# Optimization experiments

Measured on AMD Instinct MI355X. Metric: run time of the kernel, lower is better.

## Reference

```python
import jax, jax.numpy as jnp
import numpy as np

EMB = 1024  # embedding_size in the torch module


def setup_inputs() -> dict:
    key = jax.random.key(0)
    ks = jax.random.split(key, 6)
    B, N, K = 64, 256, 4096
    y = jax.random.normal(ks[0], (B, N, 1024), dtype=jnp.float32)
    # nn.Linear weights, init normal(std=0.02), zero bias
    Wy_w = jax.random.normal(ks[1], (1024, 1024), dtype=jnp.float32) * 0.02  # [out,in]
    Wy_b = jnp.zeros((1024,), dtype=jnp.float32)
    Wz_w = jax.random.normal(ks[2], (1024, 2048), dtype=jnp.float32) * 0.02  # [out,in]
    Wz_b = jnp.zeros((1024,), dtype=jnp.float32)
    dic_z = jax.random.normal(ks[3], (K, 2048), dtype=jnp.float32)
    prior = jax.random.uniform(ks[4], (K,), dtype=jnp.float32)
    prior = prior / jnp.sum(prior)
    return {"y": y, "Wy_w": Wy_w, "Wy_b": Wy_b, "Wz_w": Wz_w, "Wz_b": Wz_b,
            "dic_z": dic_z, "prior": prior}


def reference(y, Wy_w, Wy_b, Wz_w, Wz_b, dic_z, prior):
    # h = Wy(y): [B,N,1024]; dz = Wz(dic_z): [K,1024]
    h = jnp.einsum('bni,oi->bno', y, Wy_w) + Wy_b
    dz = jnp.einsum('ki,oi->ko', dic_z, Wz_w) + Wz_b
    # attention over dictionary: [B,N,K]
    att = jax.nn.softmax(jnp.einsum('bnd,kd->bnk', h, dz) / jnp.sqrt(jnp.float32(EMB)), axis=-1)
    # z[b,n] = sum_k prior[k] * att[b,n,k] * dic_z[k]  -> [B,N,2048]
    # (avoids the [B,N,K,2048] intermediate the torch code materializes)
    z = jnp.einsum('bnk,k,ke->bne', att, prior, dic_z)
    return z
```

## Files before the change

### kernel.cpp

```cpp
#include <hip/hip_runtime.h>
#include <hip/hip_bf16.h>
#include <stdint.h>

typedef __bf16 bf16;
typedef __bf16 bf16x4 __attribute__((ext_vector_type(4)));
typedef __bf16 bf16x8 __attribute__((ext_vector_type(8)));
typedef float f32x4 __attribute__((ext_vector_type(4)));
typedef unsigned short ushort8 __attribute__((ext_vector_type(8)));

__device__ __forceinline__ void gload16(const bf16* g, char* l) {
  __builtin_amdgcn_global_load_lds(
      reinterpret_cast<const __attribute__((address_space(1))) unsigned int*>(
          reinterpret_cast<uintptr_t>(g)),
      reinterpret_cast<__attribute__((address_space(3))) unsigned int*>(
          reinterpret_cast<uintptr_t>(l)),
      16, 0, 0);
}

#define VMCNT(n)  asm volatile("s_waitcnt vmcnt(" #n ")" ::: "memory")
#define LGKM0()   do { asm volatile("s_waitcnt lgkmcnt(0)" ::: "memory"); \
                       __builtin_amdgcn_sched_barrier(0); } while (0)
#define BAR()     __builtin_amdgcn_s_barrier()

#define CAST_B 2048
__global__ __launch_bounds__(256) void prep_all(
    const float* __restrict__ y, bf16* __restrict__ yo, int na,
    const float* __restrict__ wy, bf16* __restrict__ wyo, int nb,
    const float* __restrict__ wz, bf16* __restrict__ wzo, int nc,
    const float* __restrict__ dic, const float* __restrict__ prior,
    bf16* __restrict__ dicb, bf16* __restrict__ w3t) {
  __shared__ bf16 t[64][72];
  const int tid = threadIdx.x;
  if ((int)blockIdx.x < CAST_B) {
    int i = blockIdx.x * 256 + tid;
    const int stride = CAST_B * 256;
    const int tot = na + nb + nc;
    for (; i < tot; i += stride) {
      const float* src; bf16* dst; int j;
      if (i < na)            { src = y;  dst = yo;  j = i; }
      else if (i < na + nb)  { src = wy; dst = wyo; j = i - na; }
      else                   { src = wz; dst = wzo; j = i - na - nb; }
      const float4 v0 = reinterpret_cast<const float4*>(src)[j * 2];
      const float4 v1 = reinterpret_cast<const float4*>(src)[j * 2 + 1];
      bf16x8 o = { (bf16)v0.x, (bf16)v0.y, (bf16)v0.z, (bf16)v0.w,
                   (bf16)v1.x, (bf16)v1.y, (bf16)v1.z, (bf16)v1.w };
      reinterpret_cast<bf16x8*>(dst)[j] = o;
    }
  } else {
    const int KD = 4096, E = 2048;
    const int b2 = blockIdx.x - CAST_B;
    const int k0 = (b2 & 63) * 64, e0 = (b2 >> 6) * 64;
    const int er = (tid & 15) * 4;
    const int kr = tid >> 4;
#pragma unroll
    for (int p = 0; p < 4; ++p) {
      const int k = kr + p * 16;
      const float pr = prior[k0 + k];
      const float4 v = *reinterpret_cast<const float4*>(dic + (size_t)(k0 + k) * E + e0 + er);
      bf16x4 db = { (bf16)v.x, (bf16)v.y, (bf16)v.z, (bf16)v.w };
      *reinterpret_cast<bf16x4*>(dicb + (size_t)(k0 + k) * E + e0 + er) = db;
      t[er + 0][k] = (bf16)(v.x * pr);
      t[er + 1][k] = (bf16)(v.y * pr);
      t[er + 2][k] = (bf16)(v.z * pr);
      t[er + 3][k] = (bf16)(v.w * pr);
    }
    __syncthreads();
    const int e = tid >> 2, kc = (tid & 3) * 16;
    ushort8 a = *reinterpret_cast<ushort8*>(&t[e][kc]);
    ushort8 b = *reinterpret_cast<ushort8*>(&t[e][kc + 8]);
    unsigned short* dst = (unsigned short*)w3t + (size_t)(e0 + e) * KD + k0 + kc;
    *reinterpret_cast<ushort8*>(dst) = a;
    *reinterpret_cast<ushort8*>(dst + 8) = b;
  }
}

__global__ __launch_bounds__(256) void rowsum_bf16(const unsigned short* __restrict__ S,
                                                   float* __restrict__ sums) {
  const int row = blockIdx.x * 4 + (threadIdx.x >> 6);
  const int lane = threadIdx.x & 63;
  const unsigned short* r = S + (size_t)row * 4096;
  float s = 0.f;
#pragma unroll
  for (int i = 0; i < 8; ++i) {
    ushort8 v = *reinterpret_cast<const ushort8*>(r + i * 512 + lane * 8);
#pragma unroll
    for (int j = 0; j < 8; ++j) s += __uint_as_float(((unsigned)v[j]) << 16);
  }
#pragma unroll
  for (int o = 32; o; o >>= 1) s += __shfl_xor(s, o);
  if (lane == 0) sums[row] = s;
}

template <int EPI, int BN>
__device__ __forceinline__ void gemm_body(
    const bf16* __restrict__ A, const bf16* __restrict__ B,
    const float* __restrict__ aux, float* __restrict__ psum,
    void* __restrict__ Cout, int M, int N, int K, float scale, int nparts,
    int orig, int nwg, char* lds) {
  constexpr int BUFSZ = 32768 + BN * 128;
  constexpr int BOFF = 32768;
  constexpr int TM = (BN == 256) ? 128 : 64;
  constexpr int MI = TM / 16;
  constexpr int NI = 4;
  const int tid = threadIdx.x;
  const int lane = tid & 63, w = tid >> 6;

  const int gridN = N / BN;
  int wgid;
  { const int q = nwg >> 3, r = nwg & 7, x = orig & 7, rest = orig >> 3;
    wgid = (x < r ? x * (q + 1) : r * (q + 1) + (x - r) * q) + rest; }
  const int m0 = (wgid / gridN) * 256;
  const int n0 = (wgid % gridN) * BN;

  const int srow = lane >> 3;
  const int scol = ((lane & 7) ^ srow) * 8;
  const bf16* gA = A + (size_t)(m0 + w * 8 + srow) * K + scol;
  const bf16* gB = B + (size_t)(n0 + w * 8 + srow) * K + scol;

  auto stA = [&](char* dst, int u, int h) {
    gload16(gA + (size_t)(h * 128) * K + (size_t)u * 64, dst + h * 16384 + w * 1024);
    gload16(gA + (size_t)(h * 128 + 64) * K + (size_t)u * 64, dst + h * 16384 + 8192 + w * 1024);
  };
  auto stB = [&](char* dst, int u, int h) {
    gload16(gB + (size_t)(h * 128) * K + (size_t)u * 64, dst + BOFF + h * 16384 + w * 1024);
    gload16(gB + (size_t)(h * 128 + 64) * K + (size_t)u * 64, dst + BOFF + h * 16384 + 8192 + w * 1024);
  };

  const int fr = lane & 15, hi = lane >> 4;
  int wm, wn;
  if constexpr (BN == 256) { wm = w >> 2; wn = w & 3; }
  else                     { wm = w >> 1; wn = w & 1; }
  const int abase = (wm * TM + fr) * 128 + ((hi ^ (fr & 7)) << 4);
  const int bbase = BOFF + (wn * 64 + fr) * 128 + ((hi ^ (fr & 7)) << 4);
#define RD_A(b, mi, ks) (*(const bf16x8*)((b) + ((abase + (mi) * 2048) ^ ((ks) << 6))))
#define RD_B(b, ni, ks) (*(const bf16x8*)((b) + ((bbase + (ni) * 2048) ^ ((ks) << 6))))

  f32x4 acc[MI][NI] = {};
  const int NT = K >> 6;

  stA(lds, 0, 0); stA(lds, 0, 1);
  stB(lds, 0, 0);
  if constexpr (BN == 256) stB(lds, 0, 1);
  stB(lds + BUFSZ, 1, 0);
  if constexpr (BN == 256) { stB(lds + BUFSZ, 1, 1); VMCNT(4); }
  else                     { VMCNT(2); }
  BAR();

  for (int u = 0; u < NT; ++u) {
    char* b  = lds + (size_t)(u & 1) * BUFSZ;
    char* bn = lds + (size_t)((u + 1) & 1) * BUFSZ;
    bf16x8 bb[2][NI], a[2][2];
    const bool sA = (u + 1) < NT, sB = (u + 2) < NT;

    if constexpr (BN == 256) {
      a[0][0] = RD_A(b, 0, 0); a[0][1] = RD_A(b, 0, 1);
      a[1][0] = RD_A(b, 1, 0); a[1][1] = RD_A(b, 1, 1);
#pragma unroll
      for (int ni = 0; ni < NI; ++ni) { bb[0][ni] = RD_B(b, ni, 0); bb[1][ni] = RD_B(b, ni, 1); }
      if (sA) stA(bn, u + 1, 0);
      LGKM0();
#pragma unroll
      for (int m2 = 0; m2 < 2; ++m2)
#pragma unroll
        for (int ni = 0; ni < NI; ++ni) {
          acc[m2][ni] = __builtin_amdgcn_mfma_f32_16x16x32_bf16(a[m2][0], bb[0][ni], acc[m2][ni], 0, 0, 0);
          acc[m2][ni] = __builtin_amdgcn_mfma_f32_16x16x32_bf16(a[m2][1], bb[1][ni], acc[m2][ni], 0, 0, 0);
        }
      a[0][0] = RD_A(b, 2, 0); a[0][1] = RD_A(b, 2, 1);
      a[1][0] = RD_A(b, 3, 0); a[1][1] = RD_A(b, 3, 1);
      if (sA) stA(bn, u + 1, 1);
      LGKM0();
#pragma unroll
      for (int m2 = 0; m2 < 2; ++m2)
#pragma unroll
        for (int ni = 0; ni < NI; ++ni) {
          acc[2 + m2][ni] = __builtin_amdgcn_mfma_f32_16x16x32_bf16(a[m2][0], bb[0][ni], acc[2 + m2][ni], 0, 0, 0);
          acc[2 + m2][ni] = __builtin_amdgcn_mfma_f32_16x16x32_bf16(a[m2][1], bb[1][ni], acc[2 + m2][ni], 0, 0, 0);
        }
      BAR();
      a[0][0] = RD_A(b, 4, 0); a[0][1] = RD_A(b, 4, 1);
      a[1][0] = RD_A(b, 5, 0); a[1][1] = RD_A(b, 5, 1);
      if (sB) stB(b, u + 2, 0);
      LGKM0();
#pragma unroll
      for (int m2 = 0; m2 < 2; ++m2)
#pragma unroll
        for (int ni = 0; ni < NI; ++ni) {
          acc[4 + m2][ni] = __builtin_amdgcn_mfma_f32_16x16x32_bf16(a[m2][0], bb[0][ni], acc[4 + m2][ni], 0, 0, 0);
          acc[4 + m2][ni] = __builtin_amdgcn_mfma_f32_16x16x32_bf16(a[m2][1], bb[1][ni], acc[4 + m2][ni], 0, 0, 0);
        }
      a[0][0] = RD_A(b, 6, 0); a[0][1] = RD_A(b, 6, 1);
      a[1][0] = RD_A(b, 7, 0); a[1][1] = RD_A(b, 7, 1);
      if (sB) stB(b, u + 2, 1);
      if (sB) VMCNT(4); else VMCNT(0);
      LGKM0();
#pragma unroll
      for (int m2 = 0; m2 < 2; ++m2)
#pragma unroll
        for (int ni = 0; ni < NI; ++ni) {
          acc[6 + m2][ni] = __builtin_amdgcn_mfma_f32_16x16x32_bf16(a[m2][0], bb[0][ni], acc[6 + m2][ni], 0, 0, 0);
          acc[6 + m2][ni] = __builtin_amdgcn_mfma_f32_16x16x32_bf16(a[m2][1], bb[1][ni], acc[6 + m2][ni], 0, 0, 0);
        }
      BAR();
    } else {
      a[0][0] = RD_A(b, 0, 0); a[0][1] = RD_A(b, 0, 1);
      a[1][0] = RD_A(b, 1, 0); a[1][1] = RD_A(b, 1, 1);
#pragma unroll
      for (int ni = 0; ni < NI; ++ni) { bb[0][ni] = RD_B(b, ni, 0); bb[1][ni] = RD_B(b, ni, 1); }
      if (sA) { stA(bn, u + 1, 0); stA(bn, u + 1, 1); }
      LGKM0();
      __builtin_amdgcn_s_setprio(1);
#pragma unroll
      for (int m2 = 0; m2 < 2; ++m2)
#pragma unroll
        for (int ni = 0; ni < NI; ++ni) {
          acc[m2][ni] = __builtin_amdgcn_mfma_f32_16x16x32_bf16(a[m2][0], bb[0][ni], acc[m2][ni], 0, 0, 0);
          acc[m2][ni] = __builtin_amdgcn_mfma_f32_16x16x32_bf16(a[m2][1], bb[1][ni], acc[m2][ni], 0, 0, 0);
        }
      __builtin_amdgcn_s_setprio(0);
      BAR();
      a[0][0] = RD_A(b, 2, 0); a[0][1] = RD_A(b, 2, 1);
      a[1][0] = RD_A(b, 3, 0); a[1][1] = RD_A(b, 3, 1);
      if (sB) stB(b, u + 2, 0);
      if (sB) VMCNT(2); else VMCNT(0);
      LGKM0();
      __builtin_amdgcn_s_setprio(1);
#pragma unroll
      for (int m2 = 0; m2 < 2; ++m2)
#pragma unroll
        for (int ni = 0; ni < NI; ++ni) {
          acc[2 + m2][ni] = __builtin_amdgcn_mfma_f32_16x16x32_bf16(a[m2][0], bb[0][ni], acc[2 + m2][ni], 0, 0, 0);
          acc[2 + m2][ni] = __builtin_amdgcn_mfma_f32_16x16x32_bf16(a[m2][1], bb[1][ni], acc[2 + m2][ni], 0, 0, 0);
        }
      __builtin_amdgcn_s_setprio(0);
      BAR();
    }
  }
#undef RD_A
#undef RD_B

  float* lsum = (float*)lds;
  if constexpr (EPI == 2) {
    if (tid < 256) {
      const float* p = aux + (size_t)(m0 + tid) * nparts;
      float s = 0.f;
      for (int bp = 0; bp < nparts; ++bp) s += p[bp];
      lsum[tid] = s;
    }
    __syncthreads();
  }

  const int lro = hi * 4;
  if constexpr (EPI == 2) {
#pragma unroll
    for (int mi = 0; mi < MI; ++mi)
#pragma unroll
      for (int j = 0; j < 4; ++j) {
        const int lr = wm * TM + mi * 16 + lro + j;
        const float inv = 1.0f / lsum[lr];
        const size_t grow = (size_t)(m0 + lr) * N;
#pragma unroll
        for (int ni = 0; ni < NI; ++ni)
          ((float*)Cout)[grow + n0 + wn * 64 + ni * 16 + fr] = acc[mi][ni][j] * inv;
      }
  } else {
    float rs[MI][4];
    if constexpr (EPI == 1) {
#pragma unroll
      for (int mi = 0; mi < MI; ++mi)
#pragma unroll
        for (int j = 0; j < 4; ++j) rs[mi][j] = 0.f;
    }
#pragma unroll
    for (int ni = 0; ni < NI; ++ni) {
      const int gcol = n0 + wn * 64 + ni * 16 + fr;
      float bvs = 0.f;
      if constexpr (EPI == 0) bvs = aux[gcol];
#pragma unroll
      for (int mi = 0; mi < MI; ++mi) {
        const int grow = m0 + wm * TM + mi * 16 + lro;
#pragma unroll
        for (int j = 0; j < 4; ++j) {
          float c = acc[mi][ni][j] * scale + bvs;
          if constexpr (EPI == 1) { c = __expf(c); rs[mi][j] += c; }
          ((bf16*)Cout)[(size_t)(grow + j) * N + gcol] = (bf16)c;
        }
      }
    }
    if constexpr (EPI == 1) {
      if (psum != nullptr) {
        float* wsum = (float*)lds;
        __syncthreads();
#pragma unroll
        for (int mi = 0; mi < MI; ++mi)
#pragma unroll
          for (int j = 0; j < 4; ++j) {
            float s = rs[mi][j];
            s += __shfl_xor(s, 1); s += __shfl_xor(s, 2);
            s += __shfl_xor(s, 4); s += __shfl_xor(s, 8);
            if (fr == 0) wsum[wn * 256 + wm * TM + mi * 16 + lro + j] = s;
          }
        __syncthreads();
        if (tid < 256) {
          const float s = wsum[tid] + wsum[256 + tid] + wsum[512 + tid] + wsum[768 + tid];
          psum[(size_t)(m0 + tid) * 16 + (n0 >> 8)] = s;
        }
      }
    }
  }
}

template <int EPI, int BN>
__global__ __launch_bounds__(512, 2) void gemm8(
    const bf16* __restrict__ A, const bf16* __restrict__ B,
    const float* __restrict__ aux, float* __restrict__ psum,
    void* __restrict__ Cout, int M, int N, int K, float scale, int nparts) {
  extern __shared__ char lds[];
  gemm_body<EPI, BN>(A, B, aux, psum, Cout, M, N, K, scale, nparts,
                     blockIdx.x, gridDim.x, lds);
}

__global__ __launch_bounds__(512, 2) void gemm_g23(
    const bf16* __restrict__ A2, const bf16* __restrict__ B2,
    const float* __restrict__ b2, bf16* __restrict__ C2,
    const bf16* __restrict__ A3, const bf16* __restrict__ B3,
    const float* __restrict__ b3, bf16* __restrict__ C3,
    int M, int D, int E, int KD, int g2n) {
  extern __shared__ char lds[];
  if ((int)blockIdx.x < g2n)
    gemm_body<0, 256>(A2, B2, b2, nullptr, C2, M, D, D, 1.0f, 0,
                      blockIdx.x, g2n, lds);
  else
    gemm_body<0, 128>(A3, B3, b3, nullptr, C3, KD, D, E, 1.0f, 0,
                      blockIdx.x - g2n, gridDim.x - g2n, lds);
}

extern "C" void kernel_launch(void* const* d_in, const int* in_sizes, int n_in,
                              void* d_out, int out_size, void* d_ws, size_t ws_size,
                              hipStream_t stream) {
  const float* y     = (const float*)d_in[0];
  const float* Wy_w  = (const float*)d_in[1];
  const float* Wy_b  = (const float*)d_in[2];
  const float* Wz_w  = (const float*)d_in[3];
  const float* Wz_b  = (const float*)d_in[4];
  const float* dic   = (const float*)d_in[5];
  const float* prior = (const float*)d_in[6];
  float* z = (float*)d_out;

  const int M = 16384, D = 1024, E = 2048, KD = 4096;

  char* ws = (char*)d_ws;
  bf16* w3t  = (bf16*)(ws);
  bf16* h    = (bf16*)(ws + ((size_t)16 << 20));
  bf16* dzb  = (bf16*)(ws + ((size_t)48 << 20));
  bf16* S    = (bf16*)(ws + ((size_t)56 << 20));
  bf16* yb   = (bf16*)(ws + ((size_t)56 << 20));
  bf16* Wyb  = (bf16*)(ws + ((size_t)88 << 20));
  bf16* Wzb  = (bf16*)(ws + ((size_t)90 << 20));
  bf16* dicb = (bf16*)(ws + ((size_t)94 << 20));

  const bool fused_sum = ws_size >= ((size_t)185 << 20);
  float* psum = fused_sum ? (float*)(ws + ((size_t)184 << 20)) : nullptr;
  float* sums = (float*)(ws + ((size_t)16 << 20));

  prep_all<<<CAST_B + 2048, 256, 0, stream>>>(
      y, yb, M * D / 8, Wy_w, Wyb, D * D / 8, Wz_w, Wzb, D * E / 8,
      dic, prior, dicb, w3t);
  {
    const int g2n = (M / 256) * (D / 256);
    const int g3n = (KD / 256) * (D / 128);
    gemm_g23<<<g2n + g3n, 512, 131072, stream>>>(
        yb, Wyb, Wy_b, h, dicb, Wzb, Wz_b, dzb, M, D, E, KD, g2n);
  }
  gemm8<1, 256><<<(M / 256) * (KD / 256), 512, 131072, stream>>>(
      h, dzb, nullptr, psum, S, M, KD, D, 0.03125f, 0);
  if (!fused_sum) {
    rowsum_bf16<<<M / 4, 256, 0, stream>>>((const unsigned short*)S, sums);
  }
  gemm8<2, 256><<<(M / 256) * (E / 256), 512, 131072, stream>>>(
      S, w3t, fused_sum ? psum : sums, nullptr, z, M, E, KD, 1.0f,
      fused_sum ? 16 : 1);
}
```

Baseline: 490.4 us.

## Triple-buffer B tiles in LDS to remove one barrier per k-step

Restructures the GEMM LDS layout so A uses a two-stage ring and B uses a separate three-stage ring indexed by u%3. B prefetches for step u+2 no longer overwrite the buffer being read, which lets the mid-iteration barrier be dropped, leaving one barrier per k-tile. It also removes the s_setprio hints in the BN=128 path. Dynamic LDS grows to 160 KB per workgroup, which stays within one workgroup per CU but adds more LDS address arithmetic (modulo 3).

```diff
diff --git a/kernel.cpp b/kernel.cpp
--- a/kernel.cpp
+++ b/kernel.cpp
@@ -97,8 +97,8 @@
     const float* __restrict__ aux, float* __restrict__ psum,
     void* __restrict__ Cout, int M, int N, int K, float scale, int nparts,
     int orig, int nwg, char* lds) {
-  constexpr int BUFSZ = 32768 + BN * 128;
-  constexpr int BOFF = 32768;
+  constexpr int BSZ = BN * 128;
+  constexpr int BBASE = 65536;
   constexpr int TM = (BN == 256) ? 128 : 64;
   constexpr int MI = TM / 16;
   constexpr int NI = 4;
@@ -117,13 +117,15 @@
   const bf16* gA = A + (size_t)(m0 + w * 8 + srow) * K + scol;
   const bf16* gB = B + (size_t)(n0 + w * 8 + srow) * K + scol;
 
-  auto stA = [&](char* dst, int u, int h) {
-    gload16(gA + (size_t)(h * 128) * K + (size_t)u * 64, dst + h * 16384 + w * 1024);
-    gload16(gA + (size_t)(h * 128 + 64) * K + (size_t)u * 64, dst + h * 16384 + 8192 + w * 1024);
+  auto stA = [&](int u, int h) {
+    char* dst = lds + (size_t)(u & 1) * 32768 + h * 16384;
+    gload16(gA + (size_t)(h * 128) * K + (size_t)u * 64, dst + w * 1024);
+    gload16(gA + (size_t)(h * 128 + 64) * K + (size_t)u * 64, dst + 8192 + w * 1024);
   };
-  auto stB = [&](char* dst, int u, int h) {
-    gload16(gB + (size_t)(h * 128) * K + (size_t)u * 64, dst + BOFF + h * 16384 + w * 1024);
-    gload16(gB + (size_t)(h * 128 + 64) * K + (size_t)u * 64, dst + BOFF + h * 16384 + 8192 + w * 1024);
+  auto stB = [&](int u, int h) {
+    char* dst = lds + BBASE + (size_t)(u % 3) * BSZ + h * 16384;
+    gload16(gB + (size_t)(h * 128) * K + (size_t)u * 64, dst + w * 1024);
+    gload16(gB + (size_t)(h * 128 + 64) * K + (size_t)u * 64, dst + 8192 + w * 1024);
   };
 
   const int fr = lane & 15, hi = lane >> 4;
@@ -131,33 +133,35 @@
   if constexpr (BN == 256) { wm = w >> 2; wn = w & 3; }
   else                     { wm = w >> 1; wn = w & 1; }
   const int abase = (wm * TM + fr) * 128 + ((hi ^ (fr & 7)) << 4);
-  const int bbase = BOFF + (wn * 64 + fr) * 128 + ((hi ^ (fr & 7)) << 4);
-#define RD_A(b, mi, ks) (*(const bf16x8*)((b) + ((abase + (mi) * 2048) ^ ((ks) << 6))))
-#define RD_B(b, ni, ks) (*(const bf16x8*)((b) + ((bbase + (ni) * 2048) ^ ((ks) << 6))))
+  const int bbase = (wn * 64 + fr) * 128 + ((hi ^ (fr & 7)) << 4);
+#define RD_A(ab, mi, ks) (*(const bf16x8*)((ab) + ((abase + (mi) * 2048) ^ ((ks) << 6))))
+#define RD_B(bp, ni, ks) (*(const bf16x8*)((bp) + ((bbase + (ni) * 2048) ^ ((ks) << 6))))
 
   f32x4 acc[MI][NI] = {};
   const int NT = K >> 6;
 
-  stA(lds, 0, 0); stA(lds, 0, 1);
-  stB(lds, 0, 0);
-  if constexpr (BN == 256) stB(lds, 0, 1);
-  stB(lds + BUFSZ, 1, 0);
-  if constexpr (BN == 256) { stB(lds + BUFSZ, 1, 1); VMCNT(4); }
-  else                     { VMCNT(2); }
+  stA(0, 0); stA(0, 1);
+  if constexpr (BN == 256) {
+    stB(0, 0); stB(0, 1); stB(1, 0); stB(1, 1);
+    VMCNT(4);
+  } else {
+    stB(0, 0); stB(1, 0);
+    VMCNT(2);
+  }
   BAR();
 
   for (int u = 0; u < NT; ++u) {
-    char* b  = lds + (size_t)(u & 1) * BUFSZ;
-    char* bn = lds + (size_t)((u + 1) & 1) * BUFSZ;
+    const char* ab = lds + (size_t)(u & 1) * 32768;
+    const char* bp = lds + BBASE + (size_t)(u % 3) * BSZ;
     bf16x8 bb[2][NI], a[2][2];
     const bool sA = (u + 1) < NT, sB = (u + 2) < NT;
 
     if constexpr (BN == 256) {
-      a[0][0] = RD_A(b, 0, 0); a[0][1] = RD_A(b, 0, 1);
-      a[1][0] = RD_A(b, 1, 0); a[1][1] = RD_A(b, 1, 1);
-#pragma unroll
-      for (int ni = 0; ni < NI; ++ni) { bb[0][ni] = RD_B(b, ni, 0); bb[1][ni] = RD_B(b, ni, 1); }
-      if (sA) stA(bn, u + 1, 0);
+      a[0][0] = RD_A(ab, 0, 0); a[0][1] = RD_A(ab, 0, 1);
+      a[1][0] = RD_A(ab, 1, 0); a[1][1] = RD_A(ab, 1, 1);
+#pragma unroll
+      for (int ni = 0; ni < NI; ++ni) { bb[0][ni] = RD_B(bp, ni, 0); bb[1][ni] = RD_B(bp, ni, 1); }
+      if (sA) stA(u + 1, 0);
       LGKM0();
 #pragma unroll
       for (int m2 = 0; m2 < 2; ++m2)
@@ -166,9 +170,9 @@
           acc[m2][ni] = __builtin_amdgcn_mfma_f32_16x16x32_bf16(a[m2][0], bb[0][ni], acc[m2][ni], 0, 0, 0);
           acc[m2][ni] = __builtin_amdgcn_mfma_f32_16x16x32_bf16(a[m2][1], bb[1][ni], acc[m2][ni], 0, 0, 0);
         }
-      a[0][0] = RD_A(b, 2, 0); a[0][1] = RD_A(b, 2, 1);
-      a[1][0] = RD_A(b, 3, 0); a[1][1] = RD_A(b, 3, 1);
-      if (sA) stA(bn, u + 1, 1);
+      a[0][0] = RD_A(ab, 2, 0); a[0][1] = RD_A(ab, 2, 1);
+      a[1][0] = RD_A(ab, 3, 0); a[1][1] = RD_A(ab, 3, 1);
+      if (sA) stA(u + 1, 1);
       LGKM0();
 #pragma unroll
       for (int m2 = 0; m2 < 2; ++m2)
@@ -177,10 +181,9 @@
           acc[2 + m2][ni] = __builtin_amdgcn_mfma_f32_16x16x32_bf16(a[m2][0], bb[0][ni], acc[2 + m2][ni], 0, 0, 0);
           acc[2 + m2][ni] = __builtin_amdgcn_mfma_f32_16x16x32_bf16(a[m2][1], bb[1][ni], acc[2 + m2][ni], 0, 0, 0);
         }
-      BAR();
-      a[0][0] = RD_A(b, 4, 0); a[0][1] = RD_A(b, 4, 1);
-      a[1][0] = RD_A(b, 5, 0); a[1][1] = RD_A(b, 5, 1);
-      if (sB) stB(b, u + 2, 0);
+      a[0][0] = RD_A(ab, 4, 0); a[0][1] = RD_A(ab, 4, 1);
+      a[1][0] = RD_A(ab, 5, 0); a[1][1] = RD_A(ab, 5, 1);
+      if (sB) stB(u + 2, 0);
       LGKM0();
 #pragma unroll
       for (int m2 = 0; m2 < 2; ++m2)
@@ -189,9 +192,9 @@
           acc[4 + m2][ni] = __builtin_amdgcn_mfma_f32_16x16x32_bf16(a[m2][0], bb[0][ni], acc[4 + m2][ni], 0, 0, 0);
           acc[4 + m2][ni] = __builtin_amdgcn_mfma_f32_16x16x32_bf16(a[m2][1], bb[1][ni], acc[4 + m2][ni], 0, 0, 0);
         }
-      a[0][0] = RD_A(b, 6, 0); a[0][1] = RD_A(b, 6, 1);
-      a[1][0] = RD_A(b, 7, 0); a[1][1] = RD_A(b, 7, 1);
-      if (sB) stB(b, u + 2, 1);
+      a[0][0] = RD_A(ab, 6, 0); a[0][1] = RD_A(ab, 6, 1);
+      a[1][0] = RD_A(ab, 7, 0); a[1][1] = RD_A(ab, 7, 1);
+      if (sB) stB(u + 2, 1);
       if (sB) VMCNT(4); else VMCNT(0);
       LGKM0();
 #pragma unroll
@@ -203,13 +206,12 @@
         }
       BAR();
     } else {
-      a[0][0] = RD_A(b, 0, 0); a[0][1] = RD_A(b, 0, 1);
-      a[1][0] = RD_A(b, 1, 0); a[1][1] = RD_A(b, 1, 1);
-#pragma unroll
-      for (int ni = 0; ni < NI; ++ni) { bb[0][ni] = RD_B(b, ni, 0); bb[1][ni] = RD_B(b, ni, 1); }
-      if (sA) { stA(bn, u + 1, 0); stA(bn, u + 1, 1); }
-      LGKM0();
-      __builtin_amdgcn_s_setprio(1);
+      a[0][0] = RD_A(ab, 0, 0); a[0][1] = RD_A(ab, 0, 1);
+      a[1][0] = RD_A(ab, 1, 0); a[1][1] = RD_A(ab, 1, 1);
+#pragma unroll
+      for (int ni = 0; ni < NI; ++ni) { bb[0][ni] = RD_B(bp, ni, 0); bb[1][ni] = RD_B(bp, ni, 1); }
+      if (sA) { stA(u + 1, 0); stA(u + 1, 1); }
+      LGKM0();
 #pragma unroll
       for (int m2 = 0; m2 < 2; ++m2)
 #pragma unroll
@@ -217,14 +219,11 @@
           acc[m2][ni] = __builtin_amdgcn_mfma_f32_16x16x32_bf16(a[m2][0], bb[0][ni], acc[m2][ni], 0, 0, 0);
           acc[m2][ni] = __builtin_amdgcn_mfma_f32_16x16x32_bf16(a[m2][1], bb[1][ni], acc[m2][ni], 0, 0, 0);
         }
-      __builtin_amdgcn_s_setprio(0);
-      BAR();
-      a[0][0] = RD_A(b, 2, 0); a[0][1] = RD_A(b, 2, 1);
-      a[1][0] = RD_A(b, 3, 0); a[1][1] = RD_A(b, 3, 1);
-      if (sB) stB(b, u + 2, 0);
+      a[0][0] = RD_A(ab, 2, 0); a[0][1] = RD_A(ab, 2, 1);
+      a[1][0] = RD_A(ab, 3, 0); a[1][1] = RD_A(ab, 3, 1);
+      if (sB) stB(u + 2, 0);
       if (sB) VMCNT(2); else VMCNT(0);
       LGKM0();
-      __builtin_amdgcn_s_setprio(1);
 #pragma unroll
       for (int m2 = 0; m2 < 2; ++m2)
 #pragma unroll
@@ -232,7 +231,6 @@
           acc[2 + m2][ni] = __builtin_amdgcn_mfma_f32_16x16x32_bf16(a[m2][0], bb[0][ni], acc[2 + m2][ni], 0, 0, 0);
           acc[2 + m2][ni] = __builtin_amdgcn_mfma_f32_16x16x32_bf16(a[m2][1], bb[1][ni], acc[2 + m2][ni], 0, 0, 0);
         }
-      __builtin_amdgcn_s_setprio(0);
       BAR();
     }
   }
@@ -244,7 +242,7 @@
     if (tid < 256) {
       const float* p = aux + (size_t)(m0 + tid) * nparts;
       float s = 0.f;
-      for (int bp = 0; bp < nparts; ++bp) s += p[bp];
+      for (int bp2 = 0; bp2 < nparts; ++bp2) s += p[bp2];
       lsum[tid] = s;
     }
     __syncthreads();
@@ -348,6 +346,7 @@
   float* z = (float*)d_out;
 
   const int M = 16384, D = 1024, E = 2048, KD = 4096;
+  const size_t LDSB = 163840;
 
   char* ws = (char*)d_ws;
   bf16* w3t  = (bf16*)(ws);
@@ -369,15 +368,15 @@
   {
     const int g2n = (M / 256) * (D / 256);
     const int g3n = (KD / 256) * (D / 128);
-    gemm_g23<<<g2n + g3n, 512, 131072, stream>>>(
+    gemm_g23<<<g2n + g3n, 512, LDSB, stream>>>(
         yb, Wyb, Wy_b, h, dicb, Wzb, Wz_b, dzb, M, D, E, KD, g2n);
   }
-  gemm8<1, 256><<<(M / 256) * (KD / 256), 512, 131072, stream>>>(
+  gemm8<1, 256><<<(M / 256) * (KD / 256), 512, LDSB, stream>>>(
       h, dzb, nullptr, psum, S, M, KD, D, 0.03125f, 0);
   if (!fused_sum) {
     rowsum_bf16<<<M / 4, 256, 0, stream>>>((const unsigned short*)S, sums);
   }
-  gemm8<2, 256><<<(M / 256) * (E / 256), 512, 131072, stream>>>(
+  gemm8<2, 256><<<(M / 256) * (E / 256), 512, LDSB, stream>>>(
       S, w3t, fused_sum ? psum : sums, nullptr, z, M, E, KD, 1.0f,
       fused_sum ? 16 : 1);
 }
```

New measurement: 490.1 us. No clear change (-0.1%).
